# Kernel tuning notes

Measured on AMD Instinct MI355X. Metric: run time of the kernel, lower is better.

## Reference

```python
import jax, jax.numpy as jnp
import numpy as np

N_ENT = 15000
N_REL = 237
HID = 128
N_STEP = 3
EPS = 1e-10
E_BASE = 200000
BATCH, NEG = 8, 16


def _lstm(x, w_ih, w_hh, b_ih, b_hh):
    # x: [T, B, H]; single-layer PyTorch-style LSTM (gate order i, f, g, o)
    B = x.shape[1]
    H = w_hh.shape[1]
    bias = b_ih + b_hh

    def step(carry, xt):
        h, c = carry
        gates = xt @ w_ih.T + h @ w_hh.T + bias  # [B, 4H]
        i, f, g, o = jnp.split(gates, 4, axis=-1)
        c = jax.nn.sigmoid(f) * c + jax.nn.sigmoid(i) * jnp.tanh(g)
        h = jax.nn.sigmoid(o) * jnp.tanh(c)
        return (h, c), h

    init = (jnp.zeros((B, H), x.dtype), jnp.zeros((B, H), x.dtype))
    _, hs = jax.lax.scan(step, init, x)
    return hs  # [T, B, H]


def setup_inputs() -> dict:
    key = jax.random.key(0)
    ks = jax.random.split(key, 16)
    h_index = jax.random.randint(ks[0], (BATCH, NEG), 0, N_ENT)
    t_index = jax.random.randint(ks[1], (BATCH, NEG), 0, N_ENT)
    r_index = jax.random.randint(ks[2], (BATCH, NEG), 0, N_REL)
    src = jax.random.randint(ks[3], (E_BASE,), 0, N_ENT)
    dst = jax.random.randint(ks[4], (E_BASE,), 0, N_ENT)
    rel = jax.random.randint(ks[5], (E_BASE,), 0, N_REL)
    edge_weight = jnp.ones((2 * E_BASE,), jnp.float32)
    s = 0.05
    query_emb = jax.random.normal(ks[6], (2 * N_REL + 1, HID), jnp.float32) * s
    w_ih = jax.random.normal(ks[7], (4 * HID, HID), jnp.float32) * s
    w_hh = jax.random.normal(ks[8], (4 * HID, HID), jnp.float32) * s
    b_ih = jax.random.normal(ks[9], (4 * HID,), jnp.float32) * s
    b_hh = jax.random.normal(ks[10], (4 * HID,), jnp.float32) * s
    weight_w = jax.random.normal(ks[11], (2 * N_REL, HID), jnp.float32) * s
    weight_b = jax.random.normal(ks[12], (2 * N_REL,), jnp.float32) * s
    lin_w = jax.random.normal(ks[13], (), jnp.float32)
    lin_b = jax.random.normal(ks[14], (), jnp.float32)
    return {"query_emb": query_emb, "w_ih": w_ih, "w_hh": w_hh, "b_ih": b_ih,
            "b_hh": b_hh, "weight_w": weight_w, "weight_b": weight_b,
            "lin_w": lin_w, "lin_b": lin_b, "edge_weight": edge_weight,
            "h_index": h_index, "t_index": t_index, "r_index": r_index,
            "src": src, "dst": dst, "rel": rel}


def reference(query_emb, w_ih, w_hh, b_ih, b_hh, weight_w, weight_b,
              lin_w, lin_b, edge_weight, h_index, t_index, r_index,
              src, dst, rel):
    R2 = 2 * N_REL
    # graph.undirected(add_inverse=True): add reversed edges with inverse relations
    node_in = jnp.concatenate([src, dst])
    node_out = jnp.concatenate([dst, src])
    relation = jnp.concatenate([rel, rel + N_REL])

    # negative_sample_to_tail
    is_t_neg = jnp.all(h_index == h_index[:, :1], axis=-1, keepdims=True)
    h_i = jnp.where(is_t_neg, h_index, t_index)
    t_i = jnp.where(is_t_neg, t_index, h_index)
    r_i = jnp.where(is_t_neg, r_index, r_index + N_REL)

    hr = (h_i * R2 + r_i).ravel()
    uniq, inv = jnp.unique(hr, return_inverse=True, size=hr.shape[0], fill_value=0)
    inv = inv.ravel().reshape(h_i.shape)
    h_set = uniq // R2
    r_set = uniq % R2
    B = uniq.shape[0]

    # query sequence: [r]*(T-1) + [end=R2]
    q_idx = jnp.concatenate([jnp.tile(r_set[None], (N_STEP - 1, 1)),
                             jnp.full((1, B), R2, r_set.dtype)], axis=0)
    query = query_emb[q_idx]                      # [T, B, H]
    hidden = _lstm(query, w_ih, w_hh, b_ih, b_hh)  # [T, B, H]

    memory = jax.nn.one_hot(h_set, N_ENT, dtype=query.dtype)[None]  # [1, B, N]
    out = None
    for i in range(N_STEP):
        k = hidden[i]                                   # [B, H]
        attn = jax.nn.softmax(jnp.einsum('bd,tbd->bt', k, hidden[:i + 1]), axis=-1)
        inp = jnp.einsum('bt,tbn->nb', attn, memory)    # [N, B]
        w = jax.nn.softmax(k @ weight_w.T + weight_b, axis=-1).T  # [R2, B]
        # gather -> relation-weight multiply -> scatter_add
        msg = inp[node_in] * w[relation] * edge_weight[:, None]   # [2E, B]
        out = jnp.zeros((N_ENT, B), inp.dtype).at[node_out].add(msg)
        out = out / jnp.maximum(out.sum(axis=0, keepdims=True), EPS)
        memory = jnp.concatenate([memory, out.T[None]], axis=0)

    score = out[t_i, inv]          # [batch, neg]
    return score * lin_w + lin_b
```

## Files before the change

kernel.cpp:

```cpp
#include <hip/hip_runtime.h>
#include <math.h>

#define N_ENT  15000
#define N_RELC 237
#define R2C    474
#define EBASE  200000
#define E2     400000
#define EPSV   1e-10f
#define CAP    72
#define NSLICE 64
#define HITCAP 65536

typedef unsigned int uint32;
typedef unsigned short ushort16;

__device__ __forceinline__ ushort16 f2bf(float x) {
    uint32 u = __float_as_uint(x);
    u = (u + 0x7FFFu + ((u >> 16) & 1u)) >> 16;
    return (ushort16)u;
}
__device__ __forceinline__ float bflo(uint32 u) { return __uint_as_float(u << 16); }
__device__ __forceinline__ float bfhi(uint32 u) { return __uint_as_float(u & 0xFFFF0000u); }
__device__ __forceinline__ uint32 pk2(float lo, float hi) {
    return (uint32)f2bf(lo) | ((uint32)f2bf(hi) << 16);
}

__global__ void init_kernel(float* __restrict__ out0, int* __restrict__ cursor,
                            float* __restrict__ Swide, int* __restrict__ misc,
                            const float* __restrict__ w_ih, const float* __restrict__ w_hh,
                            const float* __restrict__ weight_w,
                            float* __restrict__ wit, float* __restrict__ wht,
                            float* __restrict__ wwt,
                            const int* __restrict__ h_index, const int* __restrict__ t_index,
                            const int* __restrict__ r_index,
                            int* __restrict__ h_set, int* __restrict__ r_set,
                            int* __restrict__ invp, int* __restrict__ t_flat,
                            int* __restrict__ headidx) {
    if (blockIdx.x == gridDim.x - 1) {
        __shared__ int sv[128], eq[128], f_[128], uniq[128], hsh[128];
        __shared__ int isneg[8];
        __shared__ int UcntS;
        int j = threadIdx.x;
        for (int idx = j; idx < N_ENT; idx += 256) headidx[idx] = -1;
        __syncthreads();
        int hrv = 0, first = 0, rank = 0;
        if (j < 128) {
            int b = j >> 4;
            eq[j] = (h_index[j] == h_index[b * 16]) ? 1 : 0;
        }
        __syncthreads();
        if (j < 128 && (j & 15) == 0) {
            int b = j >> 4, a = 1;
            for (int q = 0; q < 16; q++) a &= eq[b * 16 + q];
            isneg[b] = a;
        }
        __syncthreads();
        if (j < 128) {
            int b = j >> 4;
            int h = h_index[j], t = t_index[j], r = r_index[j];
            int hi, ti, ri;
            if (isneg[b]) { hi = h; ti = t; ri = r; }
            else          { hi = t; ti = h; ri = r + N_RELC; }
            t_flat[j] = ti;
            hrv = hi * R2C + ri;
            sv[j] = hrv;
            uniq[j] = 0;
        }
        __syncthreads();
        if (j < 128) {
            first = 1;
            for (int q = 0; q < j; q++) if (sv[q] == hrv) { first = 0; break; }
            f_[j] = first;
        }
        __syncthreads();
        if (j < 128) {
            for (int q = 0; q < 128; q++) rank += (f_[q] && sv[q] < hrv) ? 1 : 0;
        }
        if (j == 0) {
            int c = 0;
            for (int q = 0; q < 128; q++) c += f_[q];
            UcntS = c;
        }
        __syncthreads();
        if (j < 128) {
            if (first) uniq[rank] = hrv;
            invp[j] = rank;
        }
        __syncthreads();
        if (j < 128) {
            int uv = uniq[j];
            h_set[j] = uv / R2C;
            r_set[j] = uv % R2C;
            hsh[j] = uv / R2C;
        }
        __syncthreads();
        if (j < 128) {
            int U = UcntS;
            int hs = hsh[j];
            if (j < U && (j == 0 || hsh[j - 1] != hs)) {
                int e = j + 1;
                while (e < U && hsh[e] == hs) e++;
                headidx[hs] = (j << 8) | e;
            }
        }
        return;
    }
    int idx = blockIdx.x * 256 + threadIdx.x;
    float4 z4 = make_float4(0.f, 0.f, 0.f, 0.f);
    if (idx < 480000) { ((float4*)out0)[idx] = z4; return; }
    idx -= 480000;
    if (idx < 3750) { ((int4*)cursor)[idx] = make_int4(0, 0, 0, 0); return; }
    idx -= 3750;
    if (idx < 6144) { ((float4*)Swide)[idx] = z4; return; }
    idx -= 6144;
    if (idx < 2) { ((int4*)misc)[idx] = make_int4(0, 0, 0, 0); return; }
    idx -= 2;
    if (idx < 65536) {
        int d = idx >> 9, g = idx & 511;
        wit[idx] = w_ih[g * 128 + d];
        wht[idx] = w_hh[g * 128 + d];
        return;
    }
    idx -= 65536;
    if (idx < 65536) {
        int d = idx >> 9, r = idx & 511;
        if (r < R2C) wwt[idx] = weight_w[r * 128 + d];
    }
}

__global__ void build_kernel(const float* __restrict__ query_emb,
                             const int* __restrict__ r_set,
                             const float* __restrict__ wit, const float* __restrict__ wht,
                             const float* __restrict__ b_ih, const float* __restrict__ b_hh,
                             float* __restrict__ hidden,
                             const int* __restrict__ src, const int* __restrict__ dst,
                             const int* __restrict__ rel, const float* __restrict__ ew,
                             const int* __restrict__ headidx,
                             int* __restrict__ cursor, int2* __restrict__ edata2,
                             int* __restrict__ hitcnt, int4* __restrict__ hitlist) {
    if (blockIdx.x < 128) {
        int b = blockIdx.x, g = threadIdx.x;
        __shared__ float x[128], h[128], gl[512];
        float bias = b_ih[g] + b_hh[g];
        if (g < 128) x[g] = query_emb[r_set[b] * 128 + g];
        __syncthreads();
        float p0 = 0.f, p1 = 0.f, p2 = 0.f, p3 = 0.f;
        #pragma unroll 8
        for (int d = 0; d < 128; d += 4) {
            p0 += x[d + 0] * wit[(d + 0) * 512 + g];
            p1 += x[d + 1] * wit[(d + 1) * 512 + g];
            p2 += x[d + 2] * wit[(d + 2) * 512 + g];
            p3 += x[d + 3] * wit[(d + 3) * 512 + g];
        }
        float xpA = bias + ((p0 + p1) + (p2 + p3));
        __syncthreads();
        if (g < 128) x[g] = query_emb[R2C * 128 + g];
        __syncthreads();
        p0 = p1 = p2 = p3 = 0.f;
        #pragma unroll 8
        for (int d = 0; d < 128; d += 4) {
            p0 += x[d + 0] * wit[(d + 0) * 512 + g];
            p1 += x[d + 1] * wit[(d + 1) * 512 + g];
            p2 += x[d + 2] * wit[(d + 2) * 512 + g];
            p3 += x[d + 3] * wit[(d + 3) * 512 + g];
        }
        float xpB = bias + ((p0 + p1) + (p2 + p3));
        if (g < 128) h[g] = 0.f;
        float c = 0.f;
        __syncthreads();
        for (int step = 0; step < 3; step++) {
            float a0 = 0.f, a1 = 0.f, a2 = 0.f, a3 = 0.f;
            #pragma unroll 8
            for (int d = 0; d < 128; d += 4) {
                a0 += h[d + 0] * wht[(d + 0) * 512 + g];
                a1 += h[d + 1] * wht[(d + 1) * 512 + g];
                a2 += h[d + 2] * wht[(d + 2) * 512 + g];
                a3 += h[d + 3] * wht[(d + 3) * 512 + g];
            }
            gl[g] = ((step < 2) ? xpA : xpB) + ((a0 + a1) + (a2 + a3));
            __syncthreads();
            if (g < 128) {
                float ig = gl[g], fg = gl[128 + g], gg = gl[256 + g], og = gl[384 + g];
                float si = 1.f / (1.f + expf(-ig));
                float sf = 1.f / (1.f + expf(-fg));
                float so = 1.f / (1.f + expf(-og));
                c = sf * c + si * tanhf(gg);
                float hh = so * tanhf(c);
                hidden[(step * 128 + b) * 128 + g] = hh;
                h[g] = hh;
            }
            __syncthreads();
        }
        return;
    }
    int e = (blockIdx.x - 128) * 512 + threadIdx.x;
    if (e >= E2) return;
    int ni, no, r;
    if (e < EBASE) { ni = src[e]; no = dst[e]; r = rel[e]; }
    else { int e2 = e - EBASE; ni = dst[e2]; no = src[e2]; r = rel[e2] + N_RELC; }
    float w = ew[e];
    int pos = atomicAdd(&cursor[no], 1);
    if (pos < CAP)
        edata2[no * CAP + pos] = make_int2((ni << 9) | r, __float_as_int(w));
    int hv = headidx[ni];
    if (hv >= 0) {
        int p = atomicAdd(hitcnt, 1);
        if (p < HITCAP) hitlist[p] = make_int4(no, r, hv, __float_as_int(w));
    }
}

__global__ void coef_kernel(const float* __restrict__ hidden, int step,
                            const float* __restrict__ Swide,
                            const float* __restrict__ wwt,
                            const float* __restrict__ weight_b,
                            ushort16* __restrict__ wTb, float* __restrict__ attnS) {
    int b = blockIdx.x, tid = threadIdx.x;
    __shared__ float k[128];
    __shared__ float red[256];
    __shared__ float sc[3];
    __shared__ float Ssum[2];
    __shared__ float logit[R2C];
    if (tid < 128) k[tid] = hidden[(step * 128 + b) * 128 + tid];
    __syncthreads();
    for (int t = 0; t <= step; t++) {
        float v = 0.f;
        if (tid < 128) v = k[tid] * hidden[(t * 128 + b) * 128 + tid];
        red[tid] = v;
        __syncthreads();
        for (int s2 = 128; s2 > 0; s2 >>= 1) {
            if (tid < s2) red[tid] += red[tid + s2];
            __syncthreads();
        }
        if (tid == 0) sc[t] = red[0];
        __syncthreads();
    }
    for (int t = 0; t < step; t++) {
        red[tid] = (tid < NSLICE) ? Swide[t * (NSLICE * 128) + tid * 128 + b] : 0.f;
        __syncthreads();
        for (int s2 = 128; s2 > 0; s2 >>= 1) {
            if (tid < s2) red[tid] += red[tid + s2];
            __syncthreads();
        }
        if (tid == 0) Ssum[t] = red[0];
        __syncthreads();
    }
    if (tid == 0) {
        float m = sc[0];
        for (int t2 = 1; t2 <= step; t2++) m = fmaxf(m, sc[t2]);
        float ssum = 0.f;
        float ex[3];
        for (int t2 = 0; t2 <= step; t2++) { ex[t2] = expf(sc[t2] - m); ssum += ex[t2]; }
        for (int t2 = 0; t2 <= step; t2++) {
            float a = ex[t2] / ssum;
            if (t2 > 0) a /= fmaxf(Ssum[t2 - 1], EPSV);
            attnS[b * 4 + t2] = a;
        }
    }
    for (int r = tid; r < R2C; r += 256) {
        float acc = weight_b[r];
        #pragma unroll 8
        for (int d = 0; d < 128; d++) acc += k[d] * wwt[d * 512 + r];
        logit[r] = acc;
    }
    __syncthreads();
    float m = -1e30f;
    for (int r = tid; r < R2C; r += 256) m = fmaxf(m, logit[r]);
    red[tid] = m; __syncthreads();
    for (int s2 = 128; s2 > 0; s2 >>= 1) {
        if (tid < s2) red[tid] = fmaxf(red[tid], red[tid + s2]);
        __syncthreads();
    }
    m = red[0]; __syncthreads();
    float s = 0.f;
    for (int r = tid; r < R2C; r += 256) s += expf(logit[r] - m);
    red[tid] = s; __syncthreads();
    for (int s2 = 128; s2 > 0; s2 >>= 1) {
        if (tid < s2) red[tid] += red[tid + s2];
        __syncthreads();
    }
    float invs = 1.f / red[0];
    for (int r = tid; r < R2C; r += 256)
        wTb[r * 128 + b] = f2bf(expf(logit[r] - m) * invs);
}

__global__ void step0_kernel(const int4* __restrict__ hitlist,
                             const int* __restrict__ hitcnt,
                             const ushort16* __restrict__ wTb,
                             float* __restrict__ out0, float* __restrict__ Sw0) {
    int idx = blockIdx.x * 256 + threadIdx.x;
    int cnt = *hitcnt;
    if (cnt > HITCAP) cnt = HITCAP;
    if (idx >= cnt) return;
    int4 hv = hitlist[idx];
    int no = hv.x, r = hv.y, b0 = hv.z >> 8, b1 = hv.z & 255;
    float w = __int_as_float(hv.w);
    int sl = (idx & (NSLICE - 1)) * 128;
    for (int b = b0; b < b1; b++) {
        float v = __uint_as_float(((uint32)wTb[r * 128 + b]) << 16) * w;
        atomicAdd(&out0[no * 128 + b], v);
        atomicAdd(&Sw0[sl + b], v);
    }
}

__global__ void inp_kernel(const float* __restrict__ o1, const ushort16* __restrict__ o2b,
                           int step, const float* __restrict__ attnS,
                           const int* __restrict__ h_set, ushort16* __restrict__ inpb) {
    int b = threadIdx.x;
    float a0 = attnS[b * 4 + 0];
    float a1 = attnS[b * 4 + 1];
    float a2 = (step >= 2) ? attnS[b * 4 + 2] : 0.f;
    int hs = h_set[b];
    for (int n = blockIdx.x; n < N_ENT; n += gridDim.x) {
        float v = (n == hs) ? a0 : 0.f;
        v += a1 * o1[n * 128 + b];
        if (step >= 2) v += a2 * __uint_as_float(((uint32)o2b[n * 128 + b]) << 16);
        inpb[n * 128 + b] = f2bf(v);
    }
}

template<int MODE>
__global__ void gather_kernel(const int2* __restrict__ edata2,
                              const int* __restrict__ cursor,
                              const ushort16* __restrict__ inpb,
                              const ushort16* __restrict__ wTb,
                              float* __restrict__ outf, ushort16* __restrict__ outb,
                              float* __restrict__ Sw) {
    __shared__ float sred[4][128];
    int wid = threadIdx.x >> 6;
    int lane = threadIdx.x & 63;
    int n = blockIdx.x * 4 + wid;
    int deg = cursor[n];
    if (deg > CAP) deg = CAP;
    const int2* ed = edata2 + n * CAP;
    int c2 = lane * 2;
    float ax = 0.f, ay = 0.f;
    int e = 0;
    for (; e + 4 <= deg; e += 4) {
        int2 d0 = ed[e + 0], d1 = ed[e + 1], d2 = ed[e + 2], d3 = ed[e + 3];
        uint32 i0 = *(const uint32*)(inpb + ((d0.x >> 9) << 7) + c2);
        uint32 w0 = *(const uint32*)(wTb  + ((d0.x & 511) << 7) + c2);
        uint32 i1 = *(const uint32*)(inpb + ((d1.x >> 9) << 7) + c2);
        uint32 w1 = *(const uint32*)(wTb  + ((d1.x & 511) << 7) + c2);
        uint32 i2 = *(const uint32*)(inpb + ((d2.x >> 9) << 7) + c2);
        uint32 w2 = *(const uint32*)(wTb  + ((d2.x & 511) << 7) + c2);
        uint32 i3 = *(const uint32*)(inpb + ((d3.x >> 9) << 7) + c2);
        uint32 w3 = *(const uint32*)(wTb  + ((d3.x & 511) << 7) + c2);
        float f0 = __int_as_float(d0.y), f1 = __int_as_float(d1.y);
        float f2 = __int_as_float(d2.y), f3 = __int_as_float(d3.y);
        ax += bflo(i0) * bflo(w0) * f0 + bflo(i1) * bflo(w1) * f1
            + bflo(i2) * bflo(w2) * f2 + bflo(i3) * bflo(w3) * f3;
        ay += bfhi(i0) * bfhi(w0) * f0 + bfhi(i1) * bfhi(w1) * f1
            + bfhi(i2) * bfhi(w2) * f2 + bfhi(i3) * bfhi(w3) * f3;
    }
    for (; e < deg; e++) {
        int2 edv = ed[e];
        float w = __int_as_float(edv.y);
        uint32 ia = *(const uint32*)(inpb + ((edv.x >> 9) << 7) + c2);
        uint32 wa = *(const uint32*)(wTb  + ((edv.x & 511) << 7) + c2);
        ax += bflo(ia) * bflo(wa) * w;
        ay += bfhi(ia) * bfhi(wa) * w;
    }
    if (MODE == 0) {
        *(uint32*)((ushort16*)outb + (n << 7) + c2) = pk2(ax, ay);
    } else {
        *(float2*)(outf + n * 128 + c2) = make_float2(ax, ay);
    }
    sred[wid][c2] = ax;
    sred[wid][c2 + 1] = ay;
    __syncthreads();
    if (threadIdx.x < 128) {
        float s = sred[0][threadIdx.x] + sred[1][threadIdx.x]
                + sred[2][threadIdx.x] + sred[3][threadIdx.x];
        atomicAdd(&Sw[(blockIdx.x & (NSLICE - 1)) * 128 + threadIdx.x], s);
    }
}

__global__ void score_kernel(const float* __restrict__ out2, const float* __restrict__ Swide,
                             const int* __restrict__ t_flat, const int* __restrict__ invp,
                             const float* __restrict__ lin_w, const float* __restrict__ lin_b,
                             float* __restrict__ d_out) {
    int j = threadIdx.x;
    int bb = invp[j];
    float s = 0.f;
    for (int sl = 0; sl < NSLICE; sl++)
        s += Swide[2 * (NSLICE * 128) + sl * 128 + bb];
    d_out[j] = out2[t_flat[j] * 128 + bb] / fmaxf(s, EPSV) * lin_w[0] + lin_b[0];
}

extern "C" void kernel_launch(void* const* d_in, const int* in_sizes, int n_in,
                              void* d_out, int out_size, void* d_ws, size_t ws_size,
                              hipStream_t stream) {
    const float* query_emb  = (const float*)d_in[0];
    const float* w_ih       = (const float*)d_in[1];
    const float* w_hh       = (const float*)d_in[2];
    const float* b_ih       = (const float*)d_in[3];
    const float* b_hh       = (const float*)d_in[4];
    const float* weight_w   = (const float*)d_in[5];
    const float* weight_b   = (const float*)d_in[6];
    const float* lin_w      = (const float*)d_in[7];
    const float* lin_b      = (const float*)d_in[8];
    const float* edge_weight= (const float*)d_in[9];
    const int*   h_index    = (const int*)d_in[10];
    const int*   t_index    = (const int*)d_in[11];
    const int*   r_index    = (const int*)d_in[12];
    const int*   src        = (const int*)d_in[13];
    const int*   dst        = (const int*)d_in[14];
    const int*   rel        = (const int*)d_in[15];
    float* out = (float*)d_out;

    char* ws = (char*)d_ws;
    size_t off_b = 0;
    auto alloc = [&](size_t bytes) -> void* {
        void* p = ws + off_b;
        off_b = (off_b + bytes + 255) & ~(size_t)255;
        return p;
    };
    float*    hidden  = (float*)alloc(3 * 128 * 128 * sizeof(float));
    float*    attnS   = (float*)alloc(128 * 4 * sizeof(float));
    ushort16* wTb     = (ushort16*)alloc(R2C * 128 * sizeof(ushort16));
    float*    Swide   = (float*)alloc(3 * NSLICE * 128 * sizeof(float));
    float*    wit     = (float*)alloc(512 * 128 * sizeof(float));
    float*    wht     = (float*)alloc(512 * 128 * sizeof(float));
    float*    wwt     = (float*)alloc(512 * 128 * sizeof(float));
    int*      h_set   = (int*)alloc(128 * sizeof(int));
    int*      r_set   = (int*)alloc(128 * sizeof(int));
    int*      invp    = (int*)alloc(128 * sizeof(int));
    int*      t_flat  = (int*)alloc(128 * sizeof(int));
    int*      cursor  = (int*)alloc(N_ENT * sizeof(int));
    int*      headidx = (int*)alloc(N_ENT * sizeof(int));
    int*      misc    = (int*)alloc(8 * sizeof(int));
    int2*     edata2  = (int2*)alloc((size_t)N_ENT * CAP * sizeof(int2));
    ushort16* inpb    = (ushort16*)alloc((size_t)N_ENT * 128 * sizeof(ushort16));
    float*    outs0   = (float*)alloc((size_t)N_ENT * 128 * sizeof(float));
    ushort16* out1b   = (ushort16*)alloc((size_t)N_ENT * 128 * sizeof(ushort16));
    int4*     hitlist = (int4*)alloc((size_t)HITCAP * sizeof(int4));
    int* hitcnt = misc;

    init_kernel<<<2427, 256, 0, stream>>>(outs0, cursor, Swide, misc,
                                          w_ih, w_hh, weight_w, wit, wht, wwt,
                                          h_index, t_index, r_index,
                                          h_set, r_set, invp, t_flat, headidx);
    build_kernel<<<128 + (E2 + 511) / 512, 512, 0, stream>>>(
        query_emb, r_set, wit, wht, b_ih, b_hh, hidden,
        src, dst, rel, edge_weight, headidx, cursor, edata2, hitcnt, hitlist);

    coef_kernel<<<128, 256, 0, stream>>>(hidden, 0, Swide, wwt, weight_b, wTb, attnS);
    step0_kernel<<<HITCAP / 256, 256, 0, stream>>>(hitlist, hitcnt, wTb, outs0, Swide);

    coef_kernel<<<128, 256, 0, stream>>>(hidden, 1, Swide, wwt, weight_b, wTb, attnS);
    inp_kernel<<<2048, 128, 0, stream>>>(outs0, out1b, 1, attnS, h_set, inpb);
    gather_kernel<0><<<N_ENT / 4, 256, 0, stream>>>(edata2, cursor, inpb, wTb,
                                                    nullptr, out1b, Swide + NSLICE * 128);

    coef_kernel<<<128, 256, 0, stream>>>(hidden, 2, Swide, wwt, weight_b, wTb, attnS);
    inp_kernel<<<2048, 128, 0, stream>>>(outs0, out1b, 2, attnS, h_set, inpb);
    gather_kernel<1><<<N_ENT / 4, 256, 0, stream>>>(edata2, cursor, inpb, wTb,
                                                    outs0, nullptr, Swide + 2 * NSLICE * 128);

    score_kernel<<<1, 128, 0, stream>>>(outs0, Swide, t_flat, invp, lin_w, lin_b, out);
}
```

Baseline: 179.4 us.

## Split LSTM and edge-fill into separate kernels, cache w_hh as bf16 in LDS

The fused build kernel, which ran the LSTM blocks alongside the edge-bucketing blocks, is split into a dedicated LSTM kernel and a separate fill kernel launched one after the other. The LSTM kernel first stages the whole recurrent weight matrix into 128KB of shared memory as packed bf16 pairs, so the three recurrent steps read weights from LDS instead of global memory. This removes repeated global reads of w_hh per block, but adds a staging pass and rounds the recurrent weights to bf16. The two kernels no longer overlap, and the 128KB LDS footprint limits residency to one block per CU.

```diff
diff --git a/kernel.cpp b/kernel.cpp
--- a/kernel.cpp
+++ b/kernel.cpp
@@ -128,72 +128,80 @@
     }
 }
 
-__global__ void build_kernel(const float* __restrict__ query_emb,
-                             const int* __restrict__ r_set,
-                             const float* __restrict__ wit, const float* __restrict__ wht,
-                             const float* __restrict__ b_ih, const float* __restrict__ b_hh,
-                             float* __restrict__ hidden,
-                             const int* __restrict__ src, const int* __restrict__ dst,
-                             const int* __restrict__ rel, const float* __restrict__ ew,
-                             const int* __restrict__ headidx,
-                             int* __restrict__ cursor, int2* __restrict__ edata2,
-                             int* __restrict__ hitcnt, int4* __restrict__ hitlist) {
-    if (blockIdx.x < 128) {
-        int b = blockIdx.x, g = threadIdx.x;
-        __shared__ float x[128], h[128], gl[512];
-        float bias = b_ih[g] + b_hh[g];
-        if (g < 128) x[g] = query_emb[r_set[b] * 128 + g];
-        __syncthreads();
-        float p0 = 0.f, p1 = 0.f, p2 = 0.f, p3 = 0.f;
+__global__ void lstm_kernel(const float* __restrict__ query_emb,
+                            const int* __restrict__ r_set,
+                            const float* __restrict__ wit, const float* __restrict__ wht,
+                            const float* __restrict__ b_ih, const float* __restrict__ b_hh,
+                            float* __restrict__ hidden) {
+    __shared__ uint32 wl[32768];
+    __shared__ float x[128], h[128], gl[512];
+    int b = blockIdx.x, g = threadIdx.x;
+    for (int i = g; i < 32768; i += 512) {
+        int dd = i >> 9, gg = i & 511;
+        float lo = wht[(2 * dd) * 512 + gg];
+        float hi = wht[(2 * dd + 1) * 512 + gg];
+        wl[i] = pk2(lo, hi);
+    }
+    float bias = b_ih[g] + b_hh[g];
+    if (g < 128) x[g] = query_emb[r_set[b] * 128 + g];
+    __syncthreads();
+    float p0 = 0.f, p1 = 0.f, p2 = 0.f, p3 = 0.f;
+    #pragma unroll 8
+    for (int d = 0; d < 128; d += 4) {
+        p0 += x[d + 0] * wit[(d + 0) * 512 + g];
+        p1 += x[d + 1] * wit[(d + 1) * 512 + g];
+        p2 += x[d + 2] * wit[(d + 2) * 512 + g];
+        p3 += x[d + 3] * wit[(d + 3) * 512 + g];
+    }
+    float xpA = bias + ((p0 + p1) + (p2 + p3));
+    __syncthreads();
+    if (g < 128) x[g] = query_emb[R2C * 128 + g];
+    __syncthreads();
+    p0 = p1 = p2 = p3 = 0.f;
+    #pragma unroll 8
+    for (int d = 0; d < 128; d += 4) {
+        p0 += x[d + 0] * wit[(d + 0) * 512 + g];
+        p1 += x[d + 1] * wit[(d + 1) * 512 + g];
+        p2 += x[d + 2] * wit[(d + 2) * 512 + g];
+        p3 += x[d + 3] * wit[(d + 3) * 512 + g];
+    }
+    float xpB = bias + ((p0 + p1) + (p2 + p3));
+    if (g < 128) h[g] = 0.f;
+    float c = 0.f;
+    __syncthreads();
+    for (int step = 0; step < 3; step++) {
+        float a0 = 0.f, a1 = 0.f, a2 = 0.f, a3 = 0.f;
         #pragma unroll 8
-        for (int d = 0; d < 128; d += 4) {
-            p0 += x[d + 0] * wit[(d + 0) * 512 + g];
-            p1 += x[d + 1] * wit[(d + 1) * 512 + g];
-            p2 += x[d + 2] * wit[(d + 2) * 512 + g];
-            p3 += x[d + 3] * wit[(d + 3) * 512 + g];
-        }
-        float xpA = bias + ((p0 + p1) + (p2 + p3));
-        __syncthreads();
-        if (g < 128) x[g] = query_emb[R2C * 128 + g];
-        __syncthreads();
-        p0 = p1 = p2 = p3 = 0.f;
-        #pragma unroll 8
-        for (int d = 0; d < 128; d += 4) {
-            p0 += x[d + 0] * wit[(d + 0) * 512 + g];
-            p1 += x[d + 1] * wit[(d + 1) * 512 + g];
-            p2 += x[d + 2] * wit[(d + 2) * 512 + g];
-            p3 += x[d + 3] * wit[(d + 3) * 512 + g];
-        }
-        float xpB = bias + ((p0 + p1) + (p2 + p3));
-        if (g < 128) h[g] = 0.f;
-        float c = 0.f;
-        __syncthreads();
-        for (int step = 0; step < 3; step++) {
-            float a0 = 0.f, a1 = 0.f, a2 = 0.f, a3 = 0.f;
-            #pragma unroll 8
-            for (int d = 0; d < 128; d += 4) {
-                a0 += h[d + 0] * wht[(d + 0) * 512 + g];
-                a1 += h[d + 1] * wht[(d + 1) * 512 + g];
-                a2 += h[d + 2] * wht[(d + 2) * 512 + g];
-                a3 += h[d + 3] * wht[(d + 3) * 512 + g];
-            }
-            gl[g] = ((step < 2) ? xpA : xpB) + ((a0 + a1) + (a2 + a3));
-            __syncthreads();
-            if (g < 128) {
-                float ig = gl[g], fg = gl[128 + g], gg = gl[256 + g], og = gl[384 + g];
-                float si = 1.f / (1.f + expf(-ig));
-                float sf = 1.f / (1.f + expf(-fg));
-                float so = 1.f / (1.f + expf(-og));
-                c = sf * c + si * tanhf(gg);
-                float hh = so * tanhf(c);
-                hidden[(step * 128 + b) * 128 + g] = hh;
-                h[g] = hh;
-            }
-            __syncthreads();
-        }
-        return;
-    }
-    int e = (blockIdx.x - 128) * 512 + threadIdx.x;
+        for (int dd = 0; dd < 64; dd += 2) {
+            uint32 wA = wl[dd * 512 + g];
+            uint32 wB = wl[(dd + 1) * 512 + g];
+            a0 += h[2 * dd + 0] * bflo(wA);
+            a1 += h[2 * dd + 1] * bfhi(wA);
+            a2 += h[2 * dd + 2] * bflo(wB);
+            a3 += h[2 * dd + 3] * bfhi(wB);
+        }
+        gl[g] = ((step < 2) ? xpA : xpB) + ((a0 + a1) + (a2 + a3));
+        __syncthreads();
+        if (g < 128) {
+            float ig = gl[g], fg = gl[128 + g], gg = gl[256 + g], og = gl[384 + g];
+            float si = 1.f / (1.f + expf(-ig));
+            float sf = 1.f / (1.f + expf(-fg));
+            float so = 1.f / (1.f + expf(-og));
+            c = sf * c + si * tanhf(gg);
+            float hh = so * tanhf(c);
+            hidden[(step * 128 + b) * 128 + g] = hh;
+            h[g] = hh;
+        }
+        __syncthreads();
+    }
+}
+
+__global__ void fill_kernel(const int* __restrict__ src, const int* __restrict__ dst,
+                            const int* __restrict__ rel, const float* __restrict__ ew,
+                            const int* __restrict__ headidx,
+                            int* __restrict__ cursor, int2* __restrict__ edata2,
+                            int* __restrict__ hitcnt, int4* __restrict__ hitlist) {
+    int e = blockIdx.x * 256 + threadIdx.x;
     if (e >= E2) return;
     int ni, no, r;
     if (e < EBASE) { ni = src[e]; no = dst[e]; r = rel[e]; }
@@ -440,9 +448,10 @@
                                           w_ih, w_hh, weight_w, wit, wht, wwt,
                                           h_index, t_index, r_index,
                                           h_set, r_set, invp, t_flat, headidx);
-    build_kernel<<<128 + (E2 + 511) / 512, 512, 0, stream>>>(
-        query_emb, r_set, wit, wht, b_ih, b_hh, hidden,
-        src, dst, rel, edge_weight, headidx, cursor, edata2, hitcnt, hitlist);
+    lstm_kernel<<<128, 512, 0, stream>>>(query_emb, r_set, wit, wht, b_ih, b_hh, hidden);
+    fill_kernel<<<(E2 + 255) / 256, 256, 0, stream>>>(src, dst, rel, edge_weight,
+                                                      headidx, cursor, edata2,
+                                                      hitcnt, hitlist);
 
     coef_kernel<<<128, 256, 0, stream>>>(hidden, 0, Swide, wwt, weight_b, wTb, attnS);
     step0_kernel<<<HITCAP / 256, 256, 0, stream>>>(hitlist, hitcnt, wTb, outs0, Swide);
```

Measured after the change: 191.7 us. 1.07x slower.
